# Performance work log

Measured on AMD Instinct MI355X. Metric: run time of the kernel, lower is better.

## Reference

```python
import jax, jax.numpy as jnp
import numpy as np

N = 131072   # batch
D = 32       # num features (main subnets)
P = 32       # num interaction pairs
H_MAIN = 64  # hidden_dim_main
H_INTER = 64 # hidden_dim_inter


def setup_inputs() -> dict:
    key = jax.random.key(0)
    ks = jax.random.split(key, 7)
    X = jax.random.normal(ks[0], (N, D), dtype=jnp.float32)
    # cyclic interaction pairs (i, (i+1) % D), matching init_kwargs literal
    pairs = jnp.asarray(np.stack([np.arange(P), (np.arange(P) + 1) % D], axis=1), dtype=jnp.int32)
    # stacked ExU params for the D main subnets: log_weight [H,1] -> [D,H], bias [1] -> [D]
    log_w_main = (jax.random.normal(ks[1], (D, H_MAIN), dtype=jnp.float32) * 0.1)
    bias_main = jnp.zeros((D,), dtype=jnp.float32)
    v_main = jax.random.normal(ks[2], (D, H_MAIN), dtype=jnp.float32) / np.float32(np.sqrt(H_MAIN))
    # stacked ExU params for the P interaction subnets: log_weight [H,2], bias [2]
    log_w_inter = (jax.random.normal(ks[3], (P, H_INTER, 2), dtype=jnp.float32) * 0.1)
    bias_inter = jnp.zeros((P, 2), dtype=jnp.float32)
    v_inter = jax.random.normal(ks[4], (P, H_INTER), dtype=jnp.float32) / np.float32(np.sqrt(H_INTER))
    # final Linear(D+P, 1)
    W_final = jax.random.normal(ks[5], (D + P,), dtype=jnp.float32) / np.float32(np.sqrt(D + P))
    b_final = jnp.zeros((), dtype=jnp.float32)
    return {
        "X": X,
        "log_w_main": log_w_main,
        "bias_main": bias_main,
        "v_main": v_main,
        "log_w_inter": log_w_inter,
        "bias_inter": bias_inter,
        "v_inter": v_inter,
        "W_final": W_final,
        "b_final": b_final,
        "pairs": pairs,
    }


def reference(X, log_w_main, bias_main, v_main, log_w_inter, bias_inter, v_inter, W_final, b_final, pairs):
    # Main subnets, batched over features: ExU(1,H) is (x - b) * exp(log_w)
    h_main = jax.nn.silu((X - bias_main[None, :])[:, :, None] * jnp.exp(log_w_main)[None, :, :])  # [N,D,H]
    m_out = jnp.einsum('ndh,dh->nd', h_main, v_main)  # [N,D]
    # Interaction subnets, batched over pairs: gather the 2 columns per pair
    Xp = X[:, pairs]  # [N,P,2]
    h_int = jax.nn.silu(jnp.einsum('npc,phc->nph', Xp - bias_inter[None, :, :], jnp.exp(log_w_inter)))  # [N,P,H]
    i_out = jnp.einsum('nph,ph->np', h_int, v_inter)  # [N,P]
    Z = jnp.concatenate([m_out, i_out], axis=1)  # [N, D+P]
    out = Z @ W_final + b_final  # [N]
    return out, Z
```

## Files before the change

### kernel.cpp

```cpp
#include <hip/hip_runtime.h>

#define DD 32
#define PP 32
#define HH 64
#define TPB 256
#define ROWS 128

#define M_NE 256
#define M_LO (-8.0f)
#define M_HI (8.0f)
#define I_NE 96
#define I_LO (-6.5f)
#define I_HI (6.5f)
#define I_CELLS (I_NE * I_NE)
#define BLOCKS_PER_P (I_CELLS / TPB)

#define MAIN_BLOCKS 32
#define INTER_BLOCKS (PP * BLOCKS_PER_P)

__device__ __forceinline__ float silu_fast(float t) {
    const float LOG2E = 1.4426950408889634f;
    return t * __builtin_amdgcn_rcpf(1.f + __builtin_amdgcn_exp2f(-t * LOG2E));
}

__device__ __forceinline__ unsigned short f2bf(float f) {
    unsigned u = __float_as_uint(f);
    u += 0x7FFF + ((u >> 16) & 1);
    return (unsigned short)(u >> 16);
}

__device__ __forceinline__ float bf2f(unsigned short s) {
    return __uint_as_float((unsigned)s << 16);
}

__global__ void build_luts(const float* __restrict__ lwm,
                           const float* __restrict__ vm,
                           const float* __restrict__ lwi,
                           const float* __restrict__ vi,
                           float* __restrict__ LUTm,
                           unsigned short* __restrict__ LUTi)
{
    const float LOG2E = 1.4426950408889634f;
    __shared__ float2 sew[HH];
    __shared__ float  sv[HH];

    if (blockIdx.x < MAIN_BLOCKS) {
        const int d = blockIdx.x;
        if (threadIdx.x < HH) {
            int t = threadIdx.x;
            sew[t] = make_float2(
                __builtin_amdgcn_exp2f(lwm[d * HH + t] * LOG2E), 0.f);
            sv[t] = vm[d * HH + t];
        }
        __syncthreads();
        const float h = (M_HI - M_LO) / (float)(M_NE - 1);
        int i = threadIdx.x;
        float s = M_LO + (float)i * h;
        float acc = 0.f;
        #pragma unroll 8
        for (int k = 0; k < HH; ++k)
            acc = fmaf(silu_fast(s * sew[k].x), sv[k], acc);
        LUTm[d * M_NE + i] = acc;
    } else {
        const float h = (I_HI - I_LO) / (float)(I_NE - 1);
        const int rel = blockIdx.x - MAIN_BLOCKS;
        const int p   = rel / BLOCKS_PER_P;
        const int cip = (rel % BLOCKS_PER_P) * TPB + threadIdx.x;
        const int i   = cip / I_NE;
        const int j   = cip - i * I_NE;
        if (threadIdx.x < HH) {
            int t = threadIdx.x;
            sew[t] = make_float2(
                __builtin_amdgcn_exp2f(lwi[(p * HH + t) * 2 + 0] * LOG2E),
                __builtin_amdgcn_exp2f(lwi[(p * HH + t) * 2 + 1] * LOG2E));
            sv[t] = vi[p * HH + t];
        }
        __syncthreads();
        float c0 = I_LO + (float)i * h;
        float c1 = I_LO + (float)j * h;
        float acc = 0.f;
        #pragma unroll 8
        for (int k = 0; k < HH; ++k) {
            float a = fmaf(c0, sew[k].x, c1 * sew[k].y);
            acc = fmaf(silu_fast(a), sv[k], acc);
        }
        unsigned short ab = f2bf(acc);
        unsigned short* cb = LUTi + (size_t)p * I_CELLS * 4;
        if (i < I_NE - 1 && j < I_NE - 1) cb[((i    ) * I_NE + j    ) * 4 + 0] = ab;
        if (i < I_NE - 1 && j > 0)        cb[((i    ) * I_NE + j - 1) * 4 + 1] = ab;
        if (i > 0        && j < I_NE - 1) cb[((i - 1) * I_NE + j    ) * 4 + 2] = ab;
        if (i > 0        && j > 0)        cb[((i - 1) * I_NE + j - 1) * 4 + 3] = ab;
    }
}

__global__ __launch_bounds__(TPB, 2) void qgam_main(
    const float* __restrict__ X,
    const float* __restrict__ bias_main,
    const float* __restrict__ bias_inter,
    const float* __restrict__ W_final,
    const float* __restrict__ b_final,
    const int* __restrict__ pairs,
    const float* __restrict__ LUTm,
    const ushort4* __restrict__ LUTi,
    float* __restrict__ out,
    float* __restrict__ Zout,
    int nrows)
{
    const float M_INVH = (float)(M_NE - 1) / (M_HI - M_LO);
    const float I_INVH = (float)(I_NE - 1) / (I_HI - I_LO);

    __shared__ float s_lutm[DD * M_NE];
    __shared__ float s_x[DD][ROWS + 1];
    __shared__ float s_t[DD][ROWS + 1];
    __shared__ float s_dot[ROWS];
    __shared__ float s_wf[DD + PP];
    __shared__ float s_moff[DD];
    __shared__ float s_io0[PP], s_io1[PP];
    __shared__ int   s_p0[PP], s_p1[PP];

    const int tid  = threadIdx.x;
    const int base = blockIdx.x * ROWS;

    {
        const float4* __restrict__ lm4 = reinterpret_cast<const float4*>(LUTm);
        float4* __restrict__ sl4 = reinterpret_cast<float4*>(s_lutm);
        #pragma unroll
        for (int k = 0; k < 8; ++k) {
            const int fi = k * TPB + tid;
            sl4[fi] = lm4[fi];
        }
    }
    {
        const float4* __restrict__ Xv =
            reinterpret_cast<const float4*>(X) + (size_t)base * (DD / 4);
        #pragma unroll
        for (int k = 0; k < 4; ++k) {
            const int fi = k * TPB + tid;
            const int rl = fi >> 3;
            const int c  = (fi & 7) * 4;
            if (base + rl < nrows) {
                float4 v = Xv[fi];
                s_x[c + 0][rl] = v.x;
                s_x[c + 1][rl] = v.y;
                s_x[c + 2][rl] = v.z;
                s_x[c + 3][rl] = v.w;
            }
        }
    }
    if (tid < DD + PP) s_wf[tid] = W_final[tid];
    if (tid < PP) {
        s_moff[tid] = -(bias_main[tid] + M_LO) * M_INVH;
        s_io0[tid]  = -(bias_inter[2 * tid + 0] + I_LO) * I_INVH;
        s_io1[tid]  = -(bias_inter[2 * tid + 1] + I_LO) * I_INVH;
        s_p0[tid]   = pairs[2 * tid + 0];
        s_p1[tid]   = pairs[2 * tid + 1];
    }
    __syncthreads();

    const int r  = tid & (ROWS - 1);
    const int hf = tid >> 7;
    const int cb = hf * 16;
    const int n  = base + r;

    float dot = (hf == 0) ? b_final[0] : 0.f;

    #pragma unroll
    for (int k = 0; k < 16; ++k) {
        const int d = cb + k;
        float u  = fmaf(s_x[d][r], M_INVH, s_moff[d]);
        int   ii = (int)floorf(u);
        ii = ii < 0 ? 0 : (ii > M_NE - 2 ? M_NE - 2 : ii);
        float f  = u - (float)ii;
        float t0 = s_lutm[(d << 8) + ii];
        float t1 = s_lutm[(d << 8) + ii + 1];
        float zv = fmaf(f, t1 - t0, t0);
        s_t[d][r] = zv;
        dot = fmaf(zv, s_wf[d], dot);
    }

    __syncthreads();
    #pragma unroll
    for (int i = 0; i < 4; ++i) {
        const int fi   = i * TPB + tid;
        const int rowl = fi >> 3;
        const int c4   = (fi & 7) * 4;
        const int row  = base + rowl;
        if (row < nrows) {
            float4 v = make_float4(s_t[c4 + 0][rowl], s_t[c4 + 1][rowl],
                                   s_t[c4 + 2][rowl], s_t[c4 + 3][rowl]);
            *reinterpret_cast<float4*>(&Zout[(size_t)row * (DD + PP) + c4]) = v;
        }
    }
    __syncthreads();

    ushort4 cell[16];
    float   fu[16], fv[16];
    #pragma unroll
    for (int k = 0; k < 16; ++k) {
        const int p = cb + k;
        float u  = fmaf(s_x[s_p0[p]][r], I_INVH, s_io0[p]);
        float v_ = fmaf(s_x[s_p1[p]][r], I_INVH, s_io1[p]);
        int   iu = (int)floorf(u);
        int   iv = (int)floorf(v_);
        iu = iu < 0 ? 0 : (iu > I_NE - 2 ? I_NE - 2 : iu);
        iv = iv < 0 ? 0 : (iv > I_NE - 2 ? I_NE - 2 : iv);
        fu[k] = u  - (float)iu;
        fv[k] = v_ - (float)iv;
        cell[k] = LUTi[(size_t)p * I_CELLS + iu * I_NE + iv];
    }
    #pragma unroll
    for (int k = 0; k < 16; ++k) {
        const int p = cb + k;
        float a00 = bf2f(cell[k].x), a01 = bf2f(cell[k].y);
        float a10 = bf2f(cell[k].z), a11 = bf2f(cell[k].w);
        float r0 = fmaf(fv[k], a01 - a00, a00);
        float r1 = fmaf(fv[k], a11 - a10, a10);
        float zv = fmaf(fu[k], r1 - r0, r0);
        s_t[p][r] = zv;
        dot = fmaf(zv, s_wf[DD + p], dot);
    }
    if (hf == 1) s_dot[r] = dot;

    __syncthreads();
    if (hf == 0 && n < nrows) out[n] = dot + s_dot[r];

    #pragma unroll
    for (int i = 0; i < 4; ++i) {
        const int fi   = i * TPB + tid;
        const int rowl = fi >> 3;
        const int c4   = (fi & 7) * 4;
        const int row  = base + rowl;
        if (row < nrows) {
            float4 v = make_float4(s_t[c4 + 0][rowl], s_t[c4 + 1][rowl],
                                   s_t[c4 + 2][rowl], s_t[c4 + 3][rowl]);
            *reinterpret_cast<float4*>(&Zout[(size_t)row * (DD + PP) + DD + c4]) = v;
        }
    }
}

extern "C" void kernel_launch(void* const* d_in, const int* in_sizes, int n_in,
                              void* d_out, int out_size, void* d_ws, size_t ws_size,
                              hipStream_t stream) {
    const float* X   = (const float*)d_in[0];
    const float* lwm = (const float*)d_in[1];
    const float* bm  = (const float*)d_in[2];
    const float* vm  = (const float*)d_in[3];
    const float* lwi = (const float*)d_in[4];
    const float* bi  = (const float*)d_in[5];
    const float* vi  = (const float*)d_in[6];
    const float* wf  = (const float*)d_in[7];
    const float* bf  = (const float*)d_in[8];
    const int* pairs = (const int*)d_in[9];

    const int nrows = in_sizes[0] / DD;
    float* out = (float*)d_out;
    float* Z   = out + nrows;

    float*          LUTm = (float*)d_ws;
    unsigned short* LUTi = (unsigned short*)((char*)d_ws +
                           ((DD * M_NE * sizeof(float) + 255) & ~255));

    build_luts<<<MAIN_BLOCKS + INTER_BLOCKS, TPB, 0, stream>>>(lwm, vm, lwi, vi,
                                                               LUTm, LUTi);

    const int grid = (nrows + ROWS - 1) / ROWS;
    qgam_main<<<grid, TPB, 0, stream>>>(X, bm, bi, wf, bf, pairs, LUTm,
                                        (const ushort4*)LUTi, out, Z, nrows);
}
```

Baseline: 34.22 us.

## Use 512-row blocks with one row per thread and a smaller main LUT

The main kernel now processes 512 rows per block with 512 threads, each thread handling all 32 features and 32 pairs for one row. This removes the half-split reduction through shared memory and amortizes the per-block LUT load over more rows. The main LUT resolution drops from 256 to 128 entries per feature, halving its shared-memory footprint and load cost at some loss of interpolation accuracy. Shared memory per block grows because of the larger s_x and s_t, which lowers occupancy and cuts the grid to 256 blocks, and the inter-loop gathers are less unrolled, so there is less memory-level parallelism per thread.

```diff
diff --git a/kernel.cpp b/kernel.cpp
--- a/kernel.cpp
+++ b/kernel.cpp
@@ -3,19 +3,20 @@
 #define DD 32
 #define PP 32
 #define HH 64
-#define TPB 256
-#define ROWS 128
-
-#define M_NE 256
+#define TPB 512
+#define ROWS 512
+
+#define M_NE 128
 #define M_LO (-8.0f)
 #define M_HI (8.0f)
 #define I_NE 96
 #define I_LO (-6.5f)
 #define I_HI (6.5f)
 #define I_CELLS (I_NE * I_NE)
-#define BLOCKS_PER_P (I_CELLS / TPB)
-
-#define MAIN_BLOCKS 32
+
+#define BTPB 256
+#define MAIN_BLOCKS ((DD * M_NE) / BTPB)
+#define BLOCKS_PER_P (I_CELLS / BTPB)
 #define INTER_BLOCKS (PP * BLOCKS_PER_P)
 
 __device__ __forceinline__ float silu_fast(float t) {
@@ -45,27 +46,23 @@
     __shared__ float  sv[HH];
 
     if (blockIdx.x < MAIN_BLOCKS) {
-        const int d = blockIdx.x;
-        if (threadIdx.x < HH) {
-            int t = threadIdx.x;
-            sew[t] = make_float2(
-                __builtin_amdgcn_exp2f(lwm[d * HH + t] * LOG2E), 0.f);
-            sv[t] = vm[d * HH + t];
-        }
-        __syncthreads();
         const float h = (M_HI - M_LO) / (float)(M_NE - 1);
-        int i = threadIdx.x;
+        int idx = blockIdx.x * BTPB + threadIdx.x;
+        int d = idx >> 7;
+        int i = idx & (M_NE - 1);
         float s = M_LO + (float)i * h;
         float acc = 0.f;
         #pragma unroll 8
-        for (int k = 0; k < HH; ++k)
-            acc = fmaf(silu_fast(s * sew[k].x), sv[k], acc);
-        LUTm[d * M_NE + i] = acc;
+        for (int k = 0; k < HH; ++k) {
+            float w = __builtin_amdgcn_exp2f(lwm[d * HH + k] * LOG2E);
+            acc = fmaf(silu_fast(s * w), vm[d * HH + k], acc);
+        }
+        LUTm[idx] = acc;
     } else {
         const float h = (I_HI - I_LO) / (float)(I_NE - 1);
         const int rel = blockIdx.x - MAIN_BLOCKS;
         const int p   = rel / BLOCKS_PER_P;
-        const int cip = (rel % BLOCKS_PER_P) * TPB + threadIdx.x;
+        const int cip = (rel % BLOCKS_PER_P) * BTPB + threadIdx.x;
         const int i   = cip / I_NE;
         const int j   = cip - i * I_NE;
         if (threadIdx.x < HH) {
@@ -112,7 +109,6 @@
     __shared__ float s_lutm[DD * M_NE];
     __shared__ float s_x[DD][ROWS + 1];
     __shared__ float s_t[DD][ROWS + 1];
-    __shared__ float s_dot[ROWS];
     __shared__ float s_wf[DD + PP];
     __shared__ float s_moff[DD];
     __shared__ float s_io0[PP], s_io1[PP];
@@ -125,16 +121,14 @@
         const float4* __restrict__ lm4 = reinterpret_cast<const float4*>(LUTm);
         float4* __restrict__ sl4 = reinterpret_cast<float4*>(s_lutm);
         #pragma unroll
-        for (int k = 0; k < 8; ++k) {
-            const int fi = k * TPB + tid;
-            sl4[fi] = lm4[fi];
-        }
+        for (int k = 0; k < 2; ++k)
+            sl4[k * TPB + tid] = lm4[k * TPB + tid];
     }
     {
         const float4* __restrict__ Xv =
             reinterpret_cast<const float4*>(X) + (size_t)base * (DD / 4);
         #pragma unroll
-        for (int k = 0; k < 4; ++k) {
+        for (int k = 0; k < 8; ++k) {
             const int fi = k * TPB + tid;
             const int rl = fi >> 3;
             const int c  = (fi & 7) * 4;
@@ -157,22 +151,19 @@
     }
     __syncthreads();
 
-    const int r  = tid & (ROWS - 1);
-    const int hf = tid >> 7;
-    const int cb = hf * 16;
-    const int n  = base + r;
-
-    float dot = (hf == 0) ? b_final[0] : 0.f;
-
-    #pragma unroll
-    for (int k = 0; k < 16; ++k) {
-        const int d = cb + k;
+    const int r = tid;
+    const int n = base + r;
+
+    float dot = b_final[0];
+
+    #pragma unroll 4
+    for (int d = 0; d < DD; ++d) {
         float u  = fmaf(s_x[d][r], M_INVH, s_moff[d]);
         int   ii = (int)floorf(u);
         ii = ii < 0 ? 0 : (ii > M_NE - 2 ? M_NE - 2 : ii);
         float f  = u - (float)ii;
-        float t0 = s_lutm[(d << 8) + ii];
-        float t1 = s_lutm[(d << 8) + ii + 1];
+        float t0 = s_lutm[(d << 7) + ii];
+        float t1 = s_lutm[(d << 7) + ii + 1];
         float zv = fmaf(f, t1 - t0, t0);
         s_t[d][r] = zv;
         dot = fmaf(zv, s_wf[d], dot);
@@ -180,7 +171,7 @@
 
     __syncthreads();
     #pragma unroll
-    for (int i = 0; i < 4; ++i) {
+    for (int i = 0; i < 8; ++i) {
         const int fi   = i * TPB + tid;
         const int rowl = fi >> 3;
         const int c4   = (fi & 7) * 4;
@@ -193,39 +184,32 @@
     }
     __syncthreads();
 
-    ushort4 cell[16];
-    float   fu[16], fv[16];
-    #pragma unroll
-    for (int k = 0; k < 16; ++k) {
-        const int p = cb + k;
-        float u  = fmaf(s_x[s_p0[p]][r], I_INVH, s_io0[p]);
-        float v_ = fmaf(s_x[s_p1[p]][r], I_INVH, s_io1[p]);
+    #pragma unroll 2
+    for (int p = 0; p < PP; ++p) {
+        const int i0 = s_p0[p], i1 = s_p1[p];
+        float u  = fmaf(s_x[i0][r], I_INVH, s_io0[p]);
+        float v_ = fmaf(s_x[i1][r], I_INVH, s_io1[p]);
         int   iu = (int)floorf(u);
         int   iv = (int)floorf(v_);
         iu = iu < 0 ? 0 : (iu > I_NE - 2 ? I_NE - 2 : iu);
         iv = iv < 0 ? 0 : (iv > I_NE - 2 ? I_NE - 2 : iv);
-        fu[k] = u  - (float)iu;
-        fv[k] = v_ - (float)iv;
-        cell[k] = LUTi[(size_t)p * I_CELLS + iu * I_NE + iv];
-    }
-    #pragma unroll
-    for (int k = 0; k < 16; ++k) {
-        const int p = cb + k;
-        float a00 = bf2f(cell[k].x), a01 = bf2f(cell[k].y);
-        float a10 = bf2f(cell[k].z), a11 = bf2f(cell[k].w);
-        float r0 = fmaf(fv[k], a01 - a00, a00);
-        float r1 = fmaf(fv[k], a11 - a10, a10);
-        float zv = fmaf(fu[k], r1 - r0, r0);
+        float fu = u  - (float)iu;
+        float fv = v_ - (float)iv;
+        ushort4 cell = LUTi[(size_t)p * I_CELLS + iu * I_NE + iv];
+        float a00 = bf2f(cell.x), a01 = bf2f(cell.y);
+        float a10 = bf2f(cell.z), a11 = bf2f(cell.w);
+        float r0 = fmaf(fv, a01 - a00, a00);
+        float r1 = fmaf(fv, a11 - a10, a10);
+        float zv = fmaf(fu, r1 - r0, r0);
         s_t[p][r] = zv;
         dot = fmaf(zv, s_wf[DD + p], dot);
     }
-    if (hf == 1) s_dot[r] = dot;
-
-    __syncthreads();
-    if (hf == 0 && n < nrows) out[n] = dot + s_dot[r];
-
+
+    if (n < nrows) out[n] = dot;
+
+    __syncthreads();
     #pragma unroll
-    for (int i = 0; i < 4; ++i) {
+    for (int i = 0; i < 8; ++i) {
         const int fi   = i * TPB + tid;
         const int rowl = fi >> 3;
         const int c4   = (fi & 7) * 4;
@@ -260,8 +244,8 @@
     unsigned short* LUTi = (unsigned short*)((char*)d_ws +
                            ((DD * M_NE * sizeof(float) + 255) & ~255));
 
-    build_luts<<<MAIN_BLOCKS + INTER_BLOCKS, TPB, 0, stream>>>(lwm, vm, lwi, vi,
-                                                               LUTm, LUTi);
+    build_luts<<<MAIN_BLOCKS + INTER_BLOCKS, BTPB, 0, stream>>>(lwm, vm, lwi, vi,
+                                                                LUTm, LUTi);
 
     const int grid = (nrows + ROWS - 1) / ROWS;
     qgam_main<<<grid, TPB, 0, stream>>>(X, bm, bi, wf, bf, pairs, LUTm,
```

Result: no change. 33.66 us (-1.6%).

## Drop shared main LUT staging; gather paired float2 entries from global and shrink row tiles

Applied to the files above, without the earlier changes.

The main-subnet lookup table is no longer copied into shared memory by every block. It is instead stored in global memory as adjacent (t0,t1) float2 pairs at twice the resolution and gathered directly through the cache. Each block now handles 64 rows with four partitions of 8 features or pairs each, and the dot products are reduced across partitions through shared memory. This removes the 32KB per-block LDS fill and raises occupancy, at the cost of more scattered global gathers and a larger LUT build.

```diff
diff --git a/kernel.cpp b/kernel.cpp
--- a/kernel.cpp
+++ b/kernel.cpp
@@ -3,19 +3,22 @@
 #define DD 32
 #define PP 32
 #define HH 64
+
 #define TPB 256
-#define ROWS 128
-
-#define M_NE 256
+#define ROWS 64
+#define NPART 4
+
+#define M_NE 512
 #define M_LO (-8.0f)
 #define M_HI (8.0f)
 #define I_NE 96
 #define I_LO (-6.5f)
 #define I_HI (6.5f)
 #define I_CELLS (I_NE * I_NE)
-#define BLOCKS_PER_P (I_CELLS / TPB)
-
-#define MAIN_BLOCKS 32
+
+#define BTPB 256
+#define MAIN_BLOCKS ((DD * M_NE) / BTPB)
+#define BLOCKS_PER_P (I_CELLS / BTPB)
 #define INTER_BLOCKS (PP * BLOCKS_PER_P)
 
 __device__ __forceinline__ float silu_fast(float t) {
@@ -37,7 +40,7 @@
                            const float* __restrict__ vm,
                            const float* __restrict__ lwi,
                            const float* __restrict__ vi,
-                           float* __restrict__ LUTm,
+                           float2* __restrict__ LUTm2,
                            unsigned short* __restrict__ LUTi)
 {
     const float LOG2E = 1.4426950408889634f;
@@ -45,27 +48,25 @@
     __shared__ float  sv[HH];
 
     if (blockIdx.x < MAIN_BLOCKS) {
-        const int d = blockIdx.x;
-        if (threadIdx.x < HH) {
-            int t = threadIdx.x;
-            sew[t] = make_float2(
-                __builtin_amdgcn_exp2f(lwm[d * HH + t] * LOG2E), 0.f);
-            sv[t] = vm[d * HH + t];
-        }
-        __syncthreads();
         const float h = (M_HI - M_LO) / (float)(M_NE - 1);
-        int i = threadIdx.x;
+        int idx = blockIdx.x * BTPB + threadIdx.x;
+        int d = idx >> 9;
+        int i = idx & (M_NE - 1);
         float s = M_LO + (float)i * h;
         float acc = 0.f;
         #pragma unroll 8
-        for (int k = 0; k < HH; ++k)
-            acc = fmaf(silu_fast(s * sew[k].x), sv[k], acc);
-        LUTm[d * M_NE + i] = acc;
+        for (int k = 0; k < HH; ++k) {
+            float w = __builtin_amdgcn_exp2f(lwm[d * HH + k] * LOG2E);
+            acc = fmaf(silu_fast(s * w), vm[d * HH + k], acc);
+        }
+        float* bp = reinterpret_cast<float*>(LUTm2 + (d << 9));
+        if (i < M_NE - 1) bp[2 * i + 0] = acc;
+        if (i > 0)        bp[2 * (i - 1) + 1] = acc;
     } else {
         const float h = (I_HI - I_LO) / (float)(I_NE - 1);
         const int rel = blockIdx.x - MAIN_BLOCKS;
         const int p   = rel / BLOCKS_PER_P;
-        const int cip = (rel % BLOCKS_PER_P) * TPB + threadIdx.x;
+        const int cip = (rel % BLOCKS_PER_P) * BTPB + threadIdx.x;
         const int i   = cip / I_NE;
         const int j   = cip - i * I_NE;
         if (threadIdx.x < HH) {
@@ -93,14 +94,14 @@
     }
 }
 
-__global__ __launch_bounds__(TPB, 2) void qgam_main(
+__global__ __launch_bounds__(TPB, 4) void qgam_main(
     const float* __restrict__ X,
     const float* __restrict__ bias_main,
     const float* __restrict__ bias_inter,
     const float* __restrict__ W_final,
     const float* __restrict__ b_final,
     const int* __restrict__ pairs,
-    const float* __restrict__ LUTm,
+    const float2* __restrict__ LUTm2,
     const ushort4* __restrict__ LUTi,
     float* __restrict__ out,
     float* __restrict__ Zout,
@@ -109,10 +110,9 @@
     const float M_INVH = (float)(M_NE - 1) / (M_HI - M_LO);
     const float I_INVH = (float)(I_NE - 1) / (I_HI - I_LO);
 
-    __shared__ float s_lutm[DD * M_NE];
     __shared__ float s_x[DD][ROWS + 1];
     __shared__ float s_t[DD][ROWS + 1];
-    __shared__ float s_dot[ROWS];
+    __shared__ float s_dot[NPART][ROWS];
     __shared__ float s_wf[DD + PP];
     __shared__ float s_moff[DD];
     __shared__ float s_io0[PP], s_io1[PP];
@@ -122,19 +122,10 @@
     const int base = blockIdx.x * ROWS;
 
     {
-        const float4* __restrict__ lm4 = reinterpret_cast<const float4*>(LUTm);
-        float4* __restrict__ sl4 = reinterpret_cast<float4*>(s_lutm);
-        #pragma unroll
-        for (int k = 0; k < 8; ++k) {
-            const int fi = k * TPB + tid;
-            sl4[fi] = lm4[fi];
-        }
-    }
-    {
         const float4* __restrict__ Xv =
             reinterpret_cast<const float4*>(X) + (size_t)base * (DD / 4);
         #pragma unroll
-        for (int k = 0; k < 4; ++k) {
+        for (int k = 0; k < 2; ++k) {
             const int fi = k * TPB + tid;
             const int rl = fi >> 3;
             const int c  = (fi & 7) * 4;
@@ -157,30 +148,36 @@
     }
     __syncthreads();
 
-    const int r  = tid & (ROWS - 1);
-    const int hf = tid >> 7;
-    const int cb = hf * 16;
-    const int n  = base + r;
-
-    float dot = (hf == 0) ? b_final[0] : 0.f;
-
+    const int r    = tid & (ROWS - 1);
+    const int part = tid >> 6;
+    const int cb   = part * 8;
+
+    float dot = 0.f;
+
+    {
+        float2 mc[8];
+        float  mf[8];
+        #pragma unroll
+        for (int k = 0; k < 8; ++k) {
+            const int d = cb + k;
+            float u  = fmaf(s_x[d][r], M_INVH, s_moff[d]);
+            int   ii = (int)floorf(u);
+            ii = ii < 0 ? 0 : (ii > M_NE - 2 ? M_NE - 2 : ii);
+            mf[k] = u - (float)ii;
+            mc[k] = LUTm2[(d << 9) + ii];
+        }
+        #pragma unroll
+        for (int k = 0; k < 8; ++k) {
+            const int d = cb + k;
+            float zv = fmaf(mf[k], mc[k].y - mc[k].x, mc[k].x);
+            s_t[d][r] = zv;
+            dot = fmaf(zv, s_wf[d], dot);
+        }
+    }
+
+    __syncthreads();
     #pragma unroll
-    for (int k = 0; k < 16; ++k) {
-        const int d = cb + k;
-        float u  = fmaf(s_x[d][r], M_INVH, s_moff[d]);
-        int   ii = (int)floorf(u);
-        ii = ii < 0 ? 0 : (ii > M_NE - 2 ? M_NE - 2 : ii);
-        float f  = u - (float)ii;
-        float t0 = s_lutm[(d << 8) + ii];
-        float t1 = s_lutm[(d << 8) + ii + 1];
-        float zv = fmaf(f, t1 - t0, t0);
-        s_t[d][r] = zv;
-        dot = fmaf(zv, s_wf[d], dot);
-    }
-
-    __syncthreads();
-    #pragma unroll
-    for (int i = 0; i < 4; ++i) {
+    for (int i = 0; i < 2; ++i) {
         const int fi   = i * TPB + tid;
         const int rowl = fi >> 3;
         const int c4   = (fi & 7) * 4;
@@ -193,39 +190,40 @@
     }
     __syncthreads();
 
-    ushort4 cell[16];
-    float   fu[16], fv[16];
+    {
+        ushort4 cell[8];
+        float   fu[8], fv[8];
+        #pragma unroll
+        for (int k = 0; k < 8; ++k) {
+            const int p = cb + k;
+            float u  = fmaf(s_x[s_p0[p]][r], I_INVH, s_io0[p]);
+            float v_ = fmaf(s_x[s_p1[p]][r], I_INVH, s_io1[p]);
+            int   iu = (int)floorf(u);
+            int   iv = (int)floorf(v_);
+            iu = iu < 0 ? 0 : (iu > I_NE - 2 ? I_NE - 2 : iu);
+            iv = iv < 0 ? 0 : (iv > I_NE - 2 ? I_NE - 2 : iv);
+            fu[k] = u  - (float)iu;
+            fv[k] = v_ - (float)iv;
+            cell[k] = LUTi[(size_t)p * I_CELLS + iu * I_NE + iv];
+        }
+        #pragma unroll
+        for (int k = 0; k < 8; ++k) {
+            const int p = cb + k;
+            float a00 = bf2f(cell[k].x), a01 = bf2f(cell[k].y);
+            float a10 = bf2f(cell[k].z), a11 = bf2f(cell[k].w);
+            float r0 = fmaf(fv[k], a01 - a00, a00);
+            float r1 = fmaf(fv[k], a11 - a10, a10);
+            float zv = fmaf(fu[k], r1 - r0, r0);
+            s_t[p][r] = zv;
+            dot = fmaf(zv, s_wf[DD + p], dot);
+        }
+    }
+    s_dot[part][r] = dot;
+
+    __syncthreads();
+
     #pragma unroll
-    for (int k = 0; k < 16; ++k) {
-        const int p = cb + k;
-        float u  = fmaf(s_x[s_p0[p]][r], I_INVH, s_io0[p]);
-        float v_ = fmaf(s_x[s_p1[p]][r], I_INVH, s_io1[p]);
-        int   iu = (int)floorf(u);
-        int   iv = (int)floorf(v_);
-        iu = iu < 0 ? 0 : (iu > I_NE - 2 ? I_NE - 2 : iu);
-        iv = iv < 0 ? 0 : (iv > I_NE - 2 ? I_NE - 2 : iv);
-        fu[k] = u  - (float)iu;
-        fv[k] = v_ - (float)iv;
-        cell[k] = LUTi[(size_t)p * I_CELLS + iu * I_NE + iv];
-    }
-    #pragma unroll
-    for (int k = 0; k < 16; ++k) {
-        const int p = cb + k;
-        float a00 = bf2f(cell[k].x), a01 = bf2f(cell[k].y);
-        float a10 = bf2f(cell[k].z), a11 = bf2f(cell[k].w);
-        float r0 = fmaf(fv[k], a01 - a00, a00);
-        float r1 = fmaf(fv[k], a11 - a10, a10);
-        float zv = fmaf(fu[k], r1 - r0, r0);
-        s_t[p][r] = zv;
-        dot = fmaf(zv, s_wf[DD + p], dot);
-    }
-    if (hf == 1) s_dot[r] = dot;
-
-    __syncthreads();
-    if (hf == 0 && n < nrows) out[n] = dot + s_dot[r];
-
-    #pragma unroll
-    for (int i = 0; i < 4; ++i) {
+    for (int i = 0; i < 2; ++i) {
         const int fi   = i * TPB + tid;
         const int rowl = fi >> 3;
         const int c4   = (fi & 7) * 4;
@@ -235,6 +233,13 @@
                                    s_t[c4 + 2][rowl], s_t[c4 + 3][rowl]);
             *reinterpret_cast<float4*>(&Zout[(size_t)row * (DD + PP) + DD + c4]) = v;
         }
+    }
+
+    if (tid < ROWS) {
+        const int n = base + tid;
+        if (n < nrows)
+            out[n] = (s_dot[0][tid] + s_dot[1][tid]) +
+                     (s_dot[2][tid] + s_dot[3][tid]) + b_final[0];
     }
 }
 
@@ -256,14 +261,13 @@
     float* out = (float*)d_out;
     float* Z   = out + nrows;
 
-    float*          LUTm = (float*)d_ws;
-    unsigned short* LUTi = (unsigned short*)((char*)d_ws +
-                           ((DD * M_NE * sizeof(float) + 255) & ~255));
-
-    build_luts<<<MAIN_BLOCKS + INTER_BLOCKS, TPB, 0, stream>>>(lwm, vm, lwi, vi,
-                                                               LUTm, LUTi);
+    float2*         LUTm2 = (float2*)d_ws;
+    unsigned short* LUTi  = (unsigned short*)((char*)d_ws + DD * M_NE * sizeof(float2));
+
+    build_luts<<<MAIN_BLOCKS + INTER_BLOCKS, BTPB, 0, stream>>>(lwm, vm, lwi, vi,
+                                                                LUTm2, LUTi);
 
     const int grid = (nrows + ROWS - 1) / ROWS;
-    qgam_main<<<grid, TPB, 0, stream>>>(X, bm, bi, wf, bf, pairs, LUTm,
+    qgam_main<<<grid, TPB, 0, stream>>>(X, bm, bi, wf, bf, pairs, LUTm2,
                                         (const ushort4*)LUTi, out, Z, nrows);
 }
```

After: 34.21 us. Within noise of the previous version (-0.0%).
